# Kernel optimization log

Measured on AMD Instinct MI355X. Metric: run time of the kernel, lower is better.

The kernel has to match this reference:

```python
import jax, jax.numpy as jnp
import numpy as np

TEMP = 0.05
EPS = 1e-8  # F.cosine_similarity eps

def setup_inputs() -> dict:
    key = jax.random.key(0)
    k1, k2 = jax.random.split(key)
    cls = jax.random.normal(k1, (4096, 1024), dtype=jnp.float32)
    hidden = jax.random.normal(k2, (4096, 1024), dtype=jnp.float32)
    return {"cls": cls, "hidden": hidden}

def _normalize(x):
    # matches F.cosine_similarity: divide by max(||x||, eps)
    n = jnp.sqrt(jnp.sum(x * x, axis=-1, keepdims=True))
    return x / jnp.maximum(n, EPS)

def reference(cls, hidden):
    a = _normalize(cls)          # [B, H]
    b = _normalize(hidden)       # [B, H]
    sim = jnp.einsum('ih,jh->ij', a, b) / TEMP  # [B, B] cosine sims / temp
    # cross-entropy with labels = arange(B): mean(logsumexp(row) - diag)
    lse = jax.nn.logsumexp(sim, axis=-1)        # [B]
    diag = jnp.diagonal(sim)                    # [B]
    return jnp.mean(lse - diag)
```

## Files before the change

kernel.cpp:

```cpp
#include <hip/hip_runtime.h>
#include <hip/hip_bf16.h>

typedef __attribute__((ext_vector_type(8))) short bf16x8;
typedef __attribute__((ext_vector_type(4))) float f32x4;

#define B_ROWS 4096
#define H_DIM  1024
#define TEMP_INV 20.0f
#define BM 256
#define BN 128
#define BK 32
#define NT (H_DIM / BK)
#define NBM (B_ROWS / BM)
#define NBN (B_ROWS / BN)

__device__ __forceinline__ void gload_lds16(const void* g, void* l) {
  __builtin_amdgcn_global_load_lds(
      (const __attribute__((address_space(1))) void*)g,
      (__attribute__((address_space(3))) void*)l, 16, 0, 0);
}

__global__ __launch_bounds__(256) void normalize_kernel(
    const float* __restrict__ cls, const float* __restrict__ hid,
    __hip_bfloat16* __restrict__ Abf, __hip_bfloat16* __restrict__ Bbf)
{
  const int w = threadIdx.x >> 6, lane = threadIdx.x & 63;
  const int r = blockIdx.x * 4 + w;
  const int rr = r & (B_ROWS - 1);
  const float* src = ((r < B_ROWS) ? cls : hid) + (size_t)rr * H_DIM;
  __hip_bfloat16* dst = ((r < B_ROWS) ? Abf : Bbf) + (size_t)rr * H_DIM;

  float4 v[4];
  float ss = 0.f;
  #pragma unroll
  for (int j = 0; j < 4; j++) {
    v[j] = reinterpret_cast<const float4*>(src)[j * 64 + lane];
    ss += v[j].x * v[j].x + v[j].y * v[j].y + v[j].z * v[j].z + v[j].w * v[j].w;
  }
  #pragma unroll
  for (int off = 1; off < 64; off <<= 1) ss += __shfl_xor(ss, off, 64);
  const float scale = 1.0f / fmaxf(sqrtf(ss), 1e-8f);

  #pragma unroll
  for (int j = 0; j < 4; j++) {
    union { ushort4 u; __hip_bfloat16 h[4]; } o;
    o.h[0] = __float2bfloat16(v[j].x * scale);
    o.h[1] = __float2bfloat16(v[j].y * scale);
    o.h[2] = __float2bfloat16(v[j].z * scale);
    o.h[3] = __float2bfloat16(v[j].w * scale);
    reinterpret_cast<ushort4*>(dst)[j * 64 + lane] = o.u;
  }
}


#define STAGE_A(BUF, TT, C)                                                   \
  gload_lds16(Abase + (size_t)(row0 + (C) * 64 + srow) * 2048 + (TT) * 64 + scolb, \
              &As[BUF][(C) * 4096 + tid * 16])
#define STAGE_B(BUF, TT, C)                                                   \
  gload_lds16(Bbase + (size_t)(col0 + (C) * 64 + srow) * 2048 + (TT) * 64 + scolb, \
              &Bs[BUF][(C) * 4096 + tid * 16])

#define STAGE6(BUF, TT)                                                       \
  { STAGE_A(BUF, TT, 0); STAGE_A(BUF, TT, 1); STAGE_A(BUF, TT, 2);            \
    STAGE_A(BUF, TT, 3); STAGE_B(BUF, TT, 0); STAGE_B(BUF, TT, 1); }

#define RDFRAGS(BC)                                                           \
  { _Pragma("unroll") for (int mi = 0; mi < 8; mi++)                          \
      af[mi] = *(const bf16x8*)(&As[BC][rA + mi * 1024]);                     \
    _Pragma("unroll") for (int ni = 0; ni < 4; ni++)                          \
      bfr[ni] = *(const bf16x8*)(&Bs[BC][rB + ni * 1024]); }

#define MFMA32()                                                              \
  { __builtin_amdgcn_s_setprio(1);                                            \
    _Pragma("unroll") for (int mi = 0; mi < 8; mi++) {                        \
      _Pragma("unroll") for (int ni = 0; ni < 4; ni++) {                      \
        acc[mi][ni] = __builtin_amdgcn_mfma_f32_16x16x32_bf16(                \
            af[mi], bfr[ni], acc[mi][ni], 0, 0, 0); } }                       \
    __builtin_amdgcn_s_setprio(0); }

#define BARB() __builtin_amdgcn_s_barrier()

#define ITER_F(BC, BN_, T_)                                                   \
  { STAGE6(BN_, (T_) + 2); RDFRAGS(BC); MFMA32();                             \
    asm volatile("s_waitcnt vmcnt(6)" ::: "memory"); BARB(); }
#define ITER_W0(BC)                                                           \
  { RDFRAGS(BC); MFMA32();                                                    \
    asm volatile("s_waitcnt vmcnt(0)" ::: "memory"); BARB(); }
#define ITER_L(BC)                                                            \
  { RDFRAGS(BC); MFMA32(); }

__global__ __launch_bounds__(256, 2) void gemm_kernel(
    const __hip_bfloat16* __restrict__ A, const __hip_bfloat16* __restrict__ Bm,
    float* __restrict__ pp, float* __restrict__ diag)
{
  __shared__ __align__(16) char As[3][16384];
  __shared__ __align__(16) char Bs[3][8192];

  const int tid  = threadIdx.x;
  const int lane = tid & 63;
  const int w    = tid >> 6;
  const int wm   = w >> 1, wn = w & 1;

  const int fid = blockIdx.y * NBN + blockIdx.x;
  const int swz = (fid & 7) * 64 + (fid >> 3);
  const int bm = swz >> 5, bn = swz & 31;

  const long row0 = (long)bm * BM, col0 = (long)bn * BN;
  const char* Abase = (const char*)A;
  const char* Bbase = (const char*)Bm;

  const int srow  = tid >> 2;
  const int scolb = (((tid & 3) ^ ((tid >> 3) & 3)) << 4);

  const int fr  = lane & 15;
  const int xsl = ((lane >> 4) * 16) ^ ((fr & 6) << 3);
  const int rA  = (wm * 128 + fr) * 64 + xsl;
  const int rB  = (wn * 64  + fr) * 64 + xsl;

  f32x4 acc[8][4] = {};
  bf16x8 af[8], bfr[4];

  STAGE6(0, 0);
  STAGE6(1, 1);
  asm volatile("s_waitcnt vmcnt(6)" ::: "memory");
  BARB();

  #pragma unroll 1
  for (int T = 0; T < 30; T += 3) {
    ITER_F(0, 2, T);
    ITER_F(1, 0, T + 1);
    ITER_F(2, 1, T + 2);
  }
  ITER_W0(0);
  ITER_L(1);

  const bool isdiag = ((bn >> 1) == bm);
  const int g = lane >> 4;
  __syncthreads();
  float* lds_p = (float*)&As[0][0];

  #pragma unroll
  for (int m = 0; m < 8; m++) {
    const int rowb = (int)row0 + wm * 128 + m * 16 + g * 4;
    float p[4] = {0.f, 0.f, 0.f, 0.f};
    #pragma unroll
    for (int n = 0; n < 4; n++) {
      const int colb = (int)col0 + wn * 64 + n * 16 + fr;
      #pragma unroll
      for (int r = 0; r < 4; r++) {
        float sim = acc[m][n][r] * TEMP_INV;
        if (isdiag && (rowb + r == colb)) diag[rowb + r] = sim;
        p[r] += __expf(sim);
      }
    }
    #pragma unroll
    for (int r = 0; r < 4; r++) {
      float s = p[r];
      s += __shfl_xor(s, 1, 64);
      s += __shfl_xor(s, 2, 64);
      s += __shfl_xor(s, 4, 64);
      s += __shfl_xor(s, 8, 64);
      if (fr == 0)
        lds_p[wn * 256 + wm * 128 + m * 16 + g * 4 + r] = s;
    }
  }
  __syncthreads();
  {
    float s = lds_p[tid] + lds_p[256 + tid];
    pp[(size_t)bn * B_ROWS + row0 + tid] = s;
  }
}

__global__ __launch_bounds__(1024) void finalize_kernel(
    const float* __restrict__ pp, const float* __restrict__ diag,
    float* __restrict__ out)
{
  int tid = threadIdx.x;
  float acc = 0.f;
  for (int i = tid; i < B_ROWS; i += 1024) {
    float s = 0.f;
    #pragma unroll
    for (int j = 0; j < NBN; j++) s += pp[(size_t)j * B_ROWS + i];
    acc += logf(s) - diag[i];
  }
  #pragma unroll
  for (int off = 1; off < 64; off <<= 1) acc += __shfl_xor(acc, off, 64);
  __shared__ float wsum[16];
  if ((tid & 63) == 0) wsum[tid >> 6] = acc;
  __syncthreads();
  if (tid == 0) {
    float t = 0.f;
    #pragma unroll
    for (int i = 0; i < 16; i++) t += wsum[i];
    out[0] = t * (1.0f / B_ROWS);
  }
}

extern "C" void kernel_launch(void* const* d_in, const int* in_sizes, int n_in,
                              void* d_out, int out_size, void* d_ws, size_t ws_size,
                              hipStream_t stream)
{
  const float* cls = (const float*)d_in[0];
  const float* hid = (const float*)d_in[1];
  float* out = (float*)d_out;
  char* ws = (char*)d_ws;

  __hip_bfloat16* Abf = (__hip_bfloat16*)ws;
  __hip_bfloat16* Bbf = (__hip_bfloat16*)(ws + (size_t)B_ROWS * H_DIM * 2);
  float* pp   = (float*)(ws + (size_t)B_ROWS * H_DIM * 4);
  float* diag = pp + (size_t)NBN * B_ROWS;

  hipLaunchKernelGGL(normalize_kernel, dim3(2 * B_ROWS / 4), dim3(256), 0, stream,
                     cls, hid, Abf, Bbf);
  hipLaunchKernelGGL(gemm_kernel, dim3(NBN, NBM), dim3(256), 0, stream,
                     Abf, Bbf, pp, diag);
  hipLaunchKernelGGL(finalize_kernel, dim3(1), dim3(1024), 0, stream,
                     pp, diag, out);
}
```

Measured before the change: 124.4 us.

## Enlarge GEMM tile to 256x256 with 8 waves, 4-stage LDS pipeline, parallel finalize

```diff
diff --git a/kernel.cpp b/kernel.cpp
--- a/kernel.cpp
+++ b/kernel.cpp
@@ -8,11 +8,9 @@
 #define H_DIM  1024
 #define TEMP_INV 20.0f
 #define BM 256
-#define BN 128
 #define BK 32
 #define NT (H_DIM / BK)
-#define NBM (B_ROWS / BM)
-#define NBN (B_ROWS / BN)
+#define NBN (B_ROWS / BM)
 
 __device__ __forceinline__ void gload_lds16(const void* g, void* l) {
   __builtin_amdgcn_global_load_lds(
@@ -22,8 +20,10 @@
 
 __global__ __launch_bounds__(256) void normalize_kernel(
     const float* __restrict__ cls, const float* __restrict__ hid,
-    __hip_bfloat16* __restrict__ Abf, __hip_bfloat16* __restrict__ Bbf)
-{
+    __hip_bfloat16* __restrict__ Abf, __hip_bfloat16* __restrict__ Bbf,
+    float* __restrict__ out)
+{
+  if (blockIdx.x == 0 && threadIdx.x == 0) out[0] = 0.0f;
   const int w = threadIdx.x >> 6, lane = threadIdx.x & 63;
   const int r = blockIdx.x * 4 + w;
   const int rr = r & (B_ROWS - 1);
@@ -53,16 +53,15 @@
 }
 
 
-#define STAGE_A(BUF, TT, C)                                                   \
-  gload_lds16(Abase + (size_t)(row0 + (C) * 64 + srow) * 2048 + (TT) * 64 + scolb, \
-              &As[BUF][(C) * 4096 + tid * 16])
-#define STAGE_B(BUF, TT, C)                                                   \
-  gload_lds16(Bbase + (size_t)(col0 + (C) * 64 + srow) * 2048 + (TT) * 64 + scolb, \
-              &Bs[BUF][(C) * 4096 + tid * 16])
-
-#define STAGE6(BUF, TT)                                                       \
-  { STAGE_A(BUF, TT, 0); STAGE_A(BUF, TT, 1); STAGE_A(BUF, TT, 2);            \
-    STAGE_A(BUF, TT, 3); STAGE_B(BUF, TT, 0); STAGE_B(BUF, TT, 1); }
+#define STAGE4(BUF, TT)                                                       \
+  { gload_lds16(Abase + (size_t)(row0 + 0   + srow) * 2048 + (TT) * 64 + scolb, \
+                &As[BUF][tid * 16]);                                          \
+    gload_lds16(Abase + (size_t)(row0 + 128 + srow) * 2048 + (TT) * 64 + scolb, \
+                &As[BUF][8192 + tid * 16]);                                   \
+    gload_lds16(Bbase + (size_t)(col0 + 0   + srow) * 2048 + (TT) * 64 + scolb, \
+                &Bs[BUF][tid * 16]);                                          \
+    gload_lds16(Bbase + (size_t)(col0 + 128 + srow) * 2048 + (TT) * 64 + scolb, \
+                &Bs[BUF][8192 + tid * 16]); }
 
 #define RDFRAGS(BC)                                                           \
   { _Pragma("unroll") for (int mi = 0; mi < 8; mi++)                          \
@@ -80,32 +79,27 @@
 
 #define BARB() __builtin_amdgcn_s_barrier()
 
-#define ITER_F(BC, BN_, T_)                                                   \
-  { STAGE6(BN_, (T_) + 2); RDFRAGS(BC); MFMA32();                             \
-    asm volatile("s_waitcnt vmcnt(6)" ::: "memory"); BARB(); }
-#define ITER_W0(BC)                                                           \
-  { RDFRAGS(BC); MFMA32();                                                    \
-    asm volatile("s_waitcnt vmcnt(0)" ::: "memory"); BARB(); }
-#define ITER_L(BC)                                                            \
-  { RDFRAGS(BC); MFMA32(); }
-
-__global__ __launch_bounds__(256, 2) void gemm_kernel(
+#define ITER_F(T_, BC)                                                        \
+  { STAGE4((BC + 3) & 3, (T_) + 3); RDFRAGS(BC); MFMA32();                    \
+    asm volatile("s_waitcnt vmcnt(8)" ::: "memory"); BARB(); }
+
+__global__ __launch_bounds__(512, 2) void gemm_kernel(
     const __hip_bfloat16* __restrict__ A, const __hip_bfloat16* __restrict__ Bm,
     float* __restrict__ pp, float* __restrict__ diag)
 {
-  __shared__ __align__(16) char As[3][16384];
-  __shared__ __align__(16) char Bs[3][8192];
+  __shared__ __align__(16) char As[4][16384];
+  __shared__ __align__(16) char Bs[4][16384];
 
   const int tid  = threadIdx.x;
   const int lane = tid & 63;
   const int w    = tid >> 6;
-  const int wm   = w >> 1, wn = w & 1;
+  const int wm   = w >> 2, wn = w & 3;
 
   const int fid = blockIdx.y * NBN + blockIdx.x;
-  const int swz = (fid & 7) * 64 + (fid >> 3);
-  const int bm = swz >> 5, bn = swz & 31;
-
-  const long row0 = (long)bm * BM, col0 = (long)bn * BN;
+  const int swz = (fid & 7) * 32 + (fid >> 3);
+  const int bm = swz >> 4, bn = swz & 15;
+
+  const long row0 = (long)bm * BM, col0 = (long)bn * BM;
   const char* Abase = (const char*)A;
   const char* Bbase = (const char*)Bm;
 
@@ -120,21 +114,28 @@
   f32x4 acc[8][4] = {};
   bf16x8 af[8], bfr[4];
 
-  STAGE6(0, 0);
-  STAGE6(1, 1);
-  asm volatile("s_waitcnt vmcnt(6)" ::: "memory");
+  STAGE4(0, 0);
+  STAGE4(1, 1);
+  STAGE4(2, 2);
+  asm volatile("s_waitcnt vmcnt(8)" ::: "memory");
   BARB();
 
   #pragma unroll 1
-  for (int T = 0; T < 30; T += 3) {
-    ITER_F(0, 2, T);
-    ITER_F(1, 0, T + 1);
-    ITER_F(2, 1, T + 2);
-  }
-  ITER_W0(0);
-  ITER_L(1);
-
-  const bool isdiag = ((bn >> 1) == bm);
+  for (int T = 0; T < 28; T += 4) {
+    ITER_F(T,     0);
+    ITER_F(T + 1, 1);
+    ITER_F(T + 2, 2);
+    ITER_F(T + 3, 3);
+  }
+  { STAGE4(3, 31); RDFRAGS(0); MFMA32();
+    asm volatile("s_waitcnt vmcnt(8)" ::: "memory"); BARB(); }
+  { RDFRAGS(1); MFMA32();
+    asm volatile("s_waitcnt vmcnt(4)" ::: "memory"); BARB(); }
+  { RDFRAGS(2); MFMA32();
+    asm volatile("s_waitcnt vmcnt(0)" ::: "memory"); BARB(); }
+  { RDFRAGS(3); MFMA32(); }
+
+  const bool isdiag = (bm == bn);
   const int g = lane >> 4;
   __syncthreads();
   float* lds_p = (float*)&As[0][0];
@@ -165,34 +166,30 @@
     }
   }
   __syncthreads();
-  {
-    float s = lds_p[tid] + lds_p[256 + tid];
+  if (tid < 256) {
+    float s = lds_p[tid] + lds_p[256 + tid] + lds_p[512 + tid] + lds_p[768 + tid];
     pp[(size_t)bn * B_ROWS + row0 + tid] = s;
   }
 }
 
-__global__ __launch_bounds__(1024) void finalize_kernel(
+__global__ __launch_bounds__(256) void finalize_kernel(
     const float* __restrict__ pp, const float* __restrict__ diag,
     float* __restrict__ out)
 {
-  int tid = threadIdx.x;
-  float acc = 0.f;
-  for (int i = tid; i < B_ROWS; i += 1024) {
-    float s = 0.f;
-    #pragma unroll
-    for (int j = 0; j < NBN; j++) s += pp[(size_t)j * B_ROWS + i];
-    acc += logf(s) - diag[i];
-  }
+  const int tid = threadIdx.x;
+  const int i = blockIdx.x * 256 + tid;
+  float s = 0.f;
+  #pragma unroll
+  for (int j = 0; j < NBN; j++) s += pp[(size_t)j * B_ROWS + i];
+  float acc = logf(s) - diag[i];
   #pragma unroll
   for (int off = 1; off < 64; off <<= 1) acc += __shfl_xor(acc, off, 64);
-  __shared__ float wsum[16];
+  __shared__ float wsum[4];
   if ((tid & 63) == 0) wsum[tid >> 6] = acc;
   __syncthreads();
   if (tid == 0) {
-    float t = 0.f;
-    #pragma unroll
-    for (int i = 0; i < 16; i++) t += wsum[i];
-    out[0] = t * (1.0f / B_ROWS);
+    float t = wsum[0] + wsum[1] + wsum[2] + wsum[3];
+    atomicAdd(out, t * (1.0f / B_ROWS));
   }
 }
 
@@ -211,9 +208,9 @@
   float* diag = pp + (size_t)NBN * B_ROWS;
 
   hipLaunchKernelGGL(normalize_kernel, dim3(2 * B_ROWS / 4), dim3(256), 0, stream,
-                     cls, hid, Abf, Bbf);
-  hipLaunchKernelGGL(gemm_kernel, dim3(NBN, NBM), dim3(256), 0, stream,
+                     cls, hid, Abf, Bbf, out);
+  hipLaunchKernelGGL(gemm_kernel, dim3(NBN, NBN), dim3(512), 0, stream,
                      Abf, Bbf, pp, diag);
-  hipLaunchKernelGGL(finalize_kernel, dim3(1), dim3(1024), 0, stream,
+  hipLaunchKernelGGL(finalize_kernel, dim3(B_ROWS / 256), dim3(256), 0, stream,
                      pp, diag, out);
 }
```

Result: faster. 113.3 us (-8.9%).
